# Kernel tuning notes

Measured on AMD Instinct MI355X. Metric: run time of the kernel, lower is better.

The kernel has to match this reference:

```python
import jax, jax.numpy as jnp
import numpy as np

ALPHA = 0.25
GAMMA = 2.0
MARGIN = 1.0
LAMBDA_GRAPH = 0.1
N = 8192
D = 128


def setup_inputs() -> dict:
    key = jax.random.key(0)
    k1, k2, k3, k4 = jax.random.split(key, 4)
    preds = jax.random.normal(k1, (N,), dtype=jnp.float32)
    targets = jax.random.randint(k2, (N,), 0, 2).astype(jnp.float32)  # binary labels
    features = jax.random.normal(k3, (N, D), dtype=jnp.float32)
    graph_features = jax.random.normal(k4, (N, D), dtype=jnp.float32)
    return {"preds": preds, "targets": targets, "features": features,
            "graph_features": graph_features}


def _focal_loss(preds, targets):
    # numerically stable BCE-with-logits, reduction='none'
    bce = jnp.maximum(preds, 0.0) - preds * targets + jnp.log1p(jnp.exp(-jnp.abs(preds)))
    pt = jnp.exp(-bce)
    return jnp.mean(ALPHA * (1.0 - pt) ** GAMMA * bce)


def _contrastive_loss(features, labels):
    # squared pairwise distances via ||a||^2 + ||b||^2 - 2 a.b  -> [N, N]
    sqn = jnp.sum(features * features, axis=-1)
    sq = sqn[:, None] + sqn[None, :] - 2.0 * (features @ features.T)
    sq = jnp.maximum(sq, 0.0)
    # safe sqrt (gradient-safe at 0)
    pos = sq > 0.0
    dist = jnp.where(pos, jnp.sqrt(jnp.where(pos, sq, 1.0)), 0.0)
    same = labels[:, None] == labels[None, :]
    # same-label pairs: dist^2 == sq ; different: clamp(margin - dist, 0)^2
    per_pair = jnp.where(same, sq, jnp.maximum(MARGIN - dist, 0.0) ** 2)
    return jnp.mean(per_pair)  # sum / N^2


def _graph_reg_loss(graph_features):
    diff = graph_features[1:] - graph_features[:-1]
    return jnp.mean(jnp.sqrt(jnp.sum(diff * diff, axis=1)))


def reference(preds, targets, features, graph_features):
    return (_focal_loss(preds, targets)
            + _contrastive_loss(features, targets)
            + LAMBDA_GRAPH * _graph_reg_loss(graph_features))
```

## Files before the change

kernel.cpp:

```cpp
#include <hip/hip_runtime.h>
#include <hip/hip_bf16.h>


#define N_PTS 8192
#define DIM 128

typedef __bf16 bf16x8 __attribute__((ext_vector_type(8)));
typedef float f32x4 __attribute__((ext_vector_type(4)));

#define VPART_OFF 0
#define SPART_OFF 131072
#define CPART_OFF 133120
#define FPART_OFF 166400
#define GPART_OFF 166912

#define NPAIR 2080
#define NFOCAL 32
#define NGRAPH 256
#define NMAIN (NPAIR + NFOCAL + NGRAPH)

__device__ __forceinline__ bf16x8 pack8(const float4 a, const float4 b) {
    bf16x8 r;
    r[0] = (__bf16)a.x; r[1] = (__bf16)a.y; r[2] = (__bf16)a.z; r[3] = (__bf16)a.w;
    r[4] = (__bf16)b.x; r[5] = (__bf16)b.y; r[6] = (__bf16)b.z; r[7] = (__bf16)b.w;
    return r;
}
__device__ __forceinline__ float ssq8(const float4 a, const float4 b) {
    return a.x * a.x + a.y * a.y + a.z * a.z + a.w * a.w
         + b.x * b.x + b.y * b.y + b.z * b.z + b.w * b.w;
}

__global__ __launch_bounds__(256) void prep_kernel(const float* __restrict__ feat,
                                                   const float* __restrict__ targets,
                                                   float* __restrict__ vpart,
                                                   float* __restrict__ spart) {
    const int b = blockIdx.x;
    const int tid = threadIdx.x;
    __shared__ float fA[512], f1[512];
    __shared__ float sred[4][3];
    const int w = tid >> 6, lane = tid & 63;
    const float2* feat2 = reinterpret_cast<const float2*>(feat);
    float2 accA = {0.f, 0.f}, acc1 = {0.f, 0.f};
    float ssqA = 0.f, ssq1 = 0.f, n1 = 0.f;
    int r = b * 64 + w * 16;
    #pragma unroll 4
    for (int i = 0; i < 16; ++i, ++r) {
        const float2 v = feat2[r * 64 + lane];
        const float tr = targets[r];
        accA.x += v.x; accA.y += v.y;
        acc1.x += tr * v.x; acc1.y += tr * v.y;
        const float s2 = v.x * v.x + v.y * v.y;
        ssqA += s2; ssq1 += tr * s2; n1 += tr;
    }
    fA[w * 128 + 2 * lane] = accA.x; fA[w * 128 + 2 * lane + 1] = accA.y;
    f1[w * 128 + 2 * lane] = acc1.x; f1[w * 128 + 2 * lane + 1] = acc1.y;
    #pragma unroll
    for (int off = 32; off > 0; off >>= 1) {
        ssqA += __shfl_down(ssqA, off);
        ssq1 += __shfl_down(ssq1, off);
    }
    if (lane == 0) { sred[w][0] = ssqA; sred[w][1] = ssq1; sred[w][2] = n1; }
    __syncthreads();
    if (tid < 128) {
        const int d = tid;
        const float c1 = f1[d] + f1[128 + d] + f1[256 + d] + f1[384 + d];
        const float ca = fA[d] + fA[128 + d] + fA[256 + d] + fA[384 + d];
        vpart[b * 256 + tid] = ca - c1;
    } else {
        const int d = tid - 128;
        vpart[b * 256 + tid] = f1[d] + f1[128 + d] + f1[256 + d] + f1[384 + d];
    }
    if (tid == 0) {
        float4 s;
        s.x = sred[0][0] + sred[1][0] + sred[2][0] + sred[3][0];
        s.y = sred[0][1] + sred[1][1] + sred[2][1] + sred[3][1];
        s.z = sred[0][2] + sred[1][2] + sred[2][2] + sred[3][2];
        s.w = 0.f;
        *reinterpret_cast<float4*>(spart + b * 4) = s;
    }
}

template<bool DIAG>
__device__ __forceinline__ float scan_slow(const f32x4 (&acc)[4][4],
                                           const f32x4 (&sqni)[4], const f32x4 (&ti4)[4],
                                           const float (&sqnj)[4], const float (&tj4)[4],
                                           int wm, int wn, int quad, int m15) {
    float lsum = 0.f;
    #pragma unroll
    for (int tm = 0; tm < 4; ++tm) {
        #pragma unroll
        for (int tn = 0; tn < 4; ++tn) {
            const int jl = wn * 64 + tn * 16 + m15;
            #pragma unroll
            for (int e = 0; e < 4; ++e) {
                const float sq = sqni[tm][e] + sqnj[tn] - 2.f * acc[tm][tn][e];
                bool excl = (ti4[tm][e] == tj4[tn]);
                if (DIAG) {
                    const int il = wm * 64 + tm * 16 + quad * 4 + e;
                    excl = excl || (jl <= il);
                }
                if (!excl && sq < 1.f) {
                    const float d = sqrtf(fmaxf(sq, 0.f));
                    const float m = 1.f - d;
                    lsum += 2.f * m * m;
                }
            }
        }
    }
    return lsum;
}

__global__ __launch_bounds__(256, 4) void main_kernel(const float* __restrict__ feat,
                                                      const float* __restrict__ preds,
                                                      const float* __restrict__ targets,
                                                      const float* __restrict__ gfeat,
                                                      float* __restrict__ c_part,
                                                      float* __restrict__ f_part,
                                                      float* __restrict__ g_part) {
    const int bx = blockIdx.x;
    const int tid = threadIdx.x;
    const int w = tid >> 6, lane = tid & 63;

    if (bx < NPAIR) {
        const int u = bx;
        const int vv = 2079 - u;
        int k = (int)((sqrtf(8.f * (float)vv + 1.f) - 1.f) * 0.5f);
        while ((k + 1) * (k + 2) / 2 <= vv) ++k;
        while (k * (k + 1) / 2 > vv) --k;
        const int bi = 63 - k;
        const int bj = 63 - (vv - k * (k + 1) / 2);

        const int quad = lane >> 4, m15 = lane & 15;
        const int wm = w >> 1, wn = w & 1;
        const int ibase = bi * 128 + wm * 64, jbase = bj * 128 + wn * 64;

        bf16x8 afs[4], bfs[4];
        float sA[4], sB[4];
        #pragma unroll
        for (int t = 0; t < 4; ++t) {
            const float* pa = feat + (ibase + t * 16 + m15) * DIM + 8 * quad;
            const float4 a0 = *reinterpret_cast<const float4*>(pa);
            const float4 a1 = *reinterpret_cast<const float4*>(pa + 4);
            afs[t] = pack8(a0, a1);
            float s = ssq8(a0, a1);
            s += __shfl_xor(s, 16); s += __shfl_xor(s, 32);
            sA[t] = s;
            const float* pb = feat + (jbase + t * 16 + m15) * DIM + 8 * quad;
            const float4 b0 = *reinterpret_cast<const float4*>(pb);
            const float4 b1 = *reinterpret_cast<const float4*>(pb + 4);
            bfs[t] = pack8(b0, b1);
            float sb = ssq8(b0, b1);
            sb += __shfl_xor(sb, 16); sb += __shfl_xor(sb, 32);
            sB[t] = sb;
        }
        f32x4 acc[4][4];
        #pragma unroll
        for (int a = 0; a < 4; ++a)
            #pragma unroll
            for (int b = 0; b < 4; ++b) acc[a][b] = (f32x4){0.f, 0.f, 0.f, 0.f};
        #pragma unroll
        for (int tm = 0; tm < 4; ++tm)
            #pragma unroll
            for (int tn = 0; tn < 4; ++tn)
                acc[tm][tn] = __builtin_amdgcn_mfma_f32_16x16x32_bf16(
                    afs[tm], bfs[tn], acc[tm][tn], 0, 0, 0);

        float minv = 1e30f;
        #pragma unroll
        for (int tm = 0; tm < 4; ++tm) {
            #pragma unroll
            for (int e = 0; e < 4; ++e) {
                const float sa = __shfl(sA[tm], quad * 4 + e);
                #pragma unroll
                for (int tn = 0; tn < 4; ++tn)
                    minv = fminf(minv, sa + sB[tn] - 2.f * acc[tm][tn][e]);
            }
        }

        float lsum = 0.f;
        if (__any(minv < 2.f)) {
            float qi = 0.f, qj = 0.f;
            {
                const float4* ri = reinterpret_cast<const float4*>(feat + (ibase + lane) * DIM);
                const float4* rj = reinterpret_cast<const float4*>(feat + (jbase + lane) * DIM);
                #pragma unroll 8
                for (int c2 = 0; c2 < 32; ++c2) {
                    const float4 x = ri[c2]; qi += x.x * x.x + x.y * x.y + x.z * x.z + x.w * x.w;
                    const float4 y = rj[c2]; qj += y.x * y.x + y.y * y.y + y.z * y.z + y.w * y.w;
                }
            }
            f32x4 sqni[4], ti4[4];
            float sqnj[4], tj4[4];
            #pragma unroll
            for (int tm = 0; tm < 4; ++tm) {
                #pragma unroll
                for (int e = 0; e < 4; ++e) sqni[tm][e] = __shfl(qi, tm * 16 + quad * 4 + e);
                ti4[tm] = *reinterpret_cast<const f32x4*>(targets + ibase + tm * 16 + quad * 4);
            }
            #pragma unroll
            for (int tn = 0; tn < 4; ++tn) {
                sqnj[tn] = __shfl(qj, tn * 16 + m15);
                tj4[tn] = targets[jbase + tn * 16 + m15];
            }
            for (int ks = 1; ks < 4; ++ks) {
                bf16x8 af2[4], bf2[4];
                #pragma unroll
                for (int t = 0; t < 4; ++t) {
                    const float* pa = feat + (ibase + t * 16 + m15) * DIM + 8 * (quad + 4 * ks);
                    af2[t] = pack8(*reinterpret_cast<const float4*>(pa),
                                   *reinterpret_cast<const float4*>(pa + 4));
                    const float* pb = feat + (jbase + t * 16 + m15) * DIM + 8 * (quad + 4 * ks);
                    bf2[t] = pack8(*reinterpret_cast<const float4*>(pb),
                                   *reinterpret_cast<const float4*>(pb + 4));
                }
                #pragma unroll
                for (int tm = 0; tm < 4; ++tm)
                    #pragma unroll
                    for (int tn = 0; tn < 4; ++tn)
                        acc[tm][tn] = __builtin_amdgcn_mfma_f32_16x16x32_bf16(
                            af2[tm], bf2[tn], acc[tm][tn], 0, 0, 0);
            }
            lsum = (bi == bj)
                ? scan_slow<true >(acc, sqni, ti4, sqnj, tj4, wm, wn, quad, m15)
                : scan_slow<false>(acc, sqni, ti4, sqnj, tj4, wm, wn, quad, m15);
            #pragma unroll
            for (int off = 32; off > 0; off >>= 1) lsum += __shfl_down(lsum, off);
        }
        if (lane == 0) c_part[u * 4 + w] = lsum;
    } else if (bx < NPAIR + NFOCAL) {
        const int b = bx - NPAIR;
        const int i = b * 256 + tid;
        const float p = preds[i], t = targets[i];
        const float bce = fmaxf(p, 0.f) - p * t + log1pf(expf(-fabsf(p)));
        const float pt = expf(-bce);
        const float om = 1.f - pt;
        float fv = 0.25f * om * om * bce;
        #pragma unroll
        for (int off = 32; off > 0; off >>= 1) fv += __shfl_down(fv, off);
        if (lane == 0) f_part[b * 4 + w] = fv;
    } else {
        const int b = bx - NPAIR - NFOCAL;
        float ga = 0.f;
        #pragma unroll
        for (int it = 0; it < 8; ++it) {
            const int r = b * 4 + w + it * 1024;
            if (r < N_PTS - 1) {
                const float2 a = *reinterpret_cast<const float2*>(gfeat + r * DIM + lane * 2);
                const float2 bb = *reinterpret_cast<const float2*>(gfeat + (r + 1) * DIM + lane * 2);
                const float dx = bb.x - a.x, dy = bb.y - a.y;
                float s = dx * dx + dy * dy;
                #pragma unroll
                for (int off = 32; off > 0; off >>= 1) s += __shfl_down(s, off);
                if (lane == 0) ga += sqrtf(s);
            }
        }
        if (lane == 0) g_part[b * 4 + w] = ga;
    }
}

__global__ __launch_bounds__(256) void finalize_kernel(const float* __restrict__ c_part,
                                                       const float* __restrict__ f_part,
                                                       const float* __restrict__ g_part,
                                                       const float* __restrict__ vpart,
                                                       const float* __restrict__ spart,
                                                       float* __restrict__ out) {
    __shared__ double sC[4], sF[4], sG[4], sV[4], sST[4], sS1[4], sN1[4];
    const int tid = threadIdx.x;
    const int w = tid >> 6, lane = tid & 63;

    double c = 0.0;
    for (int i = tid; i < NPAIR * 4; i += 256) c += (double)c_part[i];
    double f = (tid < NFOCAL * 4) ? (double)f_part[tid] : 0.0;
    double g = 0.0;
    for (int i = tid; i < NGRAPH * 4; i += 256) g += (double)g_part[i];

    float V = 0.f;
    #pragma unroll 8
    for (int b2 = 0; b2 < 128; ++b2) V += vpart[b2 * 256 + tid];
    double vsq = (double)V * (double)V;

    double st = 0.0, s1 = 0.0, n1 = 0.0;
    if (tid < 128) {
        const float4 s = *reinterpret_cast<const float4*>(spart + tid * 4);
        st = s.x; s1 = s.y; n1 = s.z;
    }
    #pragma unroll
    for (int off = 32; off > 0; off >>= 1) {
        c += __shfl_down(c, off);
        f += __shfl_down(f, off);
        g += __shfl_down(g, off);
        vsq += __shfl_down(vsq, off);
        st += __shfl_down(st, off);
        s1 += __shfl_down(s1, off);
        n1 += __shfl_down(n1, off);
    }
    if (lane == 0) {
        sC[w] = c; sF[w] = f; sG[w] = g; sV[w] = vsq;
        sST[w] = st; sS1[w] = s1; sN1[w] = n1;
    }
    __syncthreads();
    if (tid == 0) {
        const double cs = sC[0] + sC[1] + sC[2] + sC[3];
        const double fs = sF[0] + sF[1] + sF[2] + sF[3];
        const double gs = sG[0] + sG[1] + sG[2] + sG[3];
        const double v0sq = sV[0] + sV[1];
        const double v1sq = sV[2] + sV[3];
        const double stot = sST[0] + sST[1] + sST[2] + sST[3];
        const double s1s  = sS1[0] + sS1[1] + sS1[2] + sS1[3];
        const double n1s  = sN1[0] + sN1[1] + sN1[2] + sN1[3];
        const double n0s = (double)N_PTS - n1s;
        const double s0s = stot - s1s;
        const double same = 2.0 * (n0s * s0s - v0sq) + 2.0 * (n1s * s1s - v1sq);
        out[0] = (float)((cs + same) / ((double)N_PTS * (double)N_PTS)
                         + fs / (double)N_PTS
                         + 0.1 * (gs / (double)(N_PTS - 1)));
    }
}

extern "C" void kernel_launch(void* const* d_in, const int* in_sizes, int n_in,
                              void* d_out, int out_size, void* d_ws, size_t ws_size,
                              hipStream_t stream) {
    const float* preds    = (const float*)d_in[0];
    const float* targets  = (const float*)d_in[1];
    const float* features = (const float*)d_in[2];
    const float* gfeat    = (const float*)d_in[3];
    char* ws = (char*)d_ws;
    float* vpart  = (float*)(ws + VPART_OFF);
    float* spart  = (float*)(ws + SPART_OFF);
    float* c_part = (float*)(ws + CPART_OFF);
    float* f_part = (float*)(ws + FPART_OFF);
    float* g_part = (float*)(ws + GPART_OFF);
    float* out = (float*)d_out;

    prep_kernel<<<128, 256, 0, stream>>>(features, targets, vpart, spart);
    main_kernel<<<NMAIN, 256, 0, stream>>>(features, preds, targets, gfeat,
                                           c_part, f_part, g_part);
    finalize_kernel<<<1, 256, 0, stream>>>(c_part, f_part, g_part, vpart, spart, out);
}
```

Baseline: 123.8 us.

## Fold prep into main kernel and coarsen blocks to 8 tiles each

Result: slower. 149.6 us (+20.9%).

```diff
diff --git a/kernel.cpp b/kernel.cpp
--- a/kernel.cpp
+++ b/kernel.cpp
@@ -7,17 +7,18 @@
 
 typedef __bf16 bf16x8 __attribute__((ext_vector_type(8)));
 typedef float f32x4 __attribute__((ext_vector_type(4)));
+
+#define G_PAIR 260
+#define G_PREP 32
+#define G_FOCAL 4
+#define G_GRAPH 64
+#define NMAIN (G_PAIR + G_PREP + G_FOCAL + G_GRAPH)
 
 #define VPART_OFF 0
 #define SPART_OFF 131072
 #define CPART_OFF 133120
-#define FPART_OFF 166400
-#define GPART_OFF 166912
-
-#define NPAIR 2080
-#define NFOCAL 32
-#define NGRAPH 256
-#define NMAIN (NPAIR + NFOCAL + NGRAPH)
+#define FPART_OFF 137280
+#define GPART_OFF 137344
 
 __device__ __forceinline__ bf16x8 pack8(const float4 a, const float4 b) {
     bf16x8 r;
@@ -28,56 +29,6 @@
 __device__ __forceinline__ float ssq8(const float4 a, const float4 b) {
     return a.x * a.x + a.y * a.y + a.z * a.z + a.w * a.w
          + b.x * b.x + b.y * b.y + b.z * b.z + b.w * b.w;
-}
-
-__global__ __launch_bounds__(256) void prep_kernel(const float* __restrict__ feat,
-                                                   const float* __restrict__ targets,
-                                                   float* __restrict__ vpart,
-                                                   float* __restrict__ spart) {
-    const int b = blockIdx.x;
-    const int tid = threadIdx.x;
-    __shared__ float fA[512], f1[512];
-    __shared__ float sred[4][3];
-    const int w = tid >> 6, lane = tid & 63;
-    const float2* feat2 = reinterpret_cast<const float2*>(feat);
-    float2 accA = {0.f, 0.f}, acc1 = {0.f, 0.f};
-    float ssqA = 0.f, ssq1 = 0.f, n1 = 0.f;
-    int r = b * 64 + w * 16;
-    #pragma unroll 4
-    for (int i = 0; i < 16; ++i, ++r) {
-        const float2 v = feat2[r * 64 + lane];
-        const float tr = targets[r];
-        accA.x += v.x; accA.y += v.y;
-        acc1.x += tr * v.x; acc1.y += tr * v.y;
-        const float s2 = v.x * v.x + v.y * v.y;
-        ssqA += s2; ssq1 += tr * s2; n1 += tr;
-    }
-    fA[w * 128 + 2 * lane] = accA.x; fA[w * 128 + 2 * lane + 1] = accA.y;
-    f1[w * 128 + 2 * lane] = acc1.x; f1[w * 128 + 2 * lane + 1] = acc1.y;
-    #pragma unroll
-    for (int off = 32; off > 0; off >>= 1) {
-        ssqA += __shfl_down(ssqA, off);
-        ssq1 += __shfl_down(ssq1, off);
-    }
-    if (lane == 0) { sred[w][0] = ssqA; sred[w][1] = ssq1; sred[w][2] = n1; }
-    __syncthreads();
-    if (tid < 128) {
-        const int d = tid;
-        const float c1 = f1[d] + f1[128 + d] + f1[256 + d] + f1[384 + d];
-        const float ca = fA[d] + fA[128 + d] + fA[256 + d] + fA[384 + d];
-        vpart[b * 256 + tid] = ca - c1;
-    } else {
-        const int d = tid - 128;
-        vpart[b * 256 + tid] = f1[d] + f1[128 + d] + f1[256 + d] + f1[384 + d];
-    }
-    if (tid == 0) {
-        float4 s;
-        s.x = sred[0][0] + sred[1][0] + sred[2][0] + sred[3][0];
-        s.y = sred[0][1] + sred[1][1] + sred[2][1] + sred[3][1];
-        s.z = sred[0][2] + sred[1][2] + sred[2][2] + sred[3][2];
-        s.w = 0.f;
-        *reinterpret_cast<float4*>(spart + b * 4) = s;
-    }
 }
 
 template<bool DIAG>
@@ -114,144 +65,212 @@
                                                       const float* __restrict__ preds,
                                                       const float* __restrict__ targets,
                                                       const float* __restrict__ gfeat,
+                                                      float* __restrict__ vpart,
+                                                      float* __restrict__ spart,
                                                       float* __restrict__ c_part,
                                                       float* __restrict__ f_part,
                                                       float* __restrict__ g_part) {
+    __shared__ float fA[512], f1[512];
+    __shared__ float sred[4][3];
     const int bx = blockIdx.x;
     const int tid = threadIdx.x;
     const int w = tid >> 6, lane = tid & 63;
 
-    if (bx < NPAIR) {
-        const int u = bx;
-        const int vv = 2079 - u;
-        int k = (int)((sqrtf(8.f * (float)vv + 1.f) - 1.f) * 0.5f);
-        while ((k + 1) * (k + 2) / 2 <= vv) ++k;
-        while (k * (k + 1) / 2 > vv) --k;
-        const int bi = 63 - k;
-        const int bj = 63 - (vv - k * (k + 1) / 2);
-
+    if (bx < G_PAIR) {
         const int quad = lane >> 4, m15 = lane & 15;
         const int wm = w >> 1, wn = w & 1;
-        const int ibase = bi * 128 + wm * 64, jbase = bj * 128 + wn * 64;
-
-        bf16x8 afs[4], bfs[4];
-        float sA[4], sB[4];
-        #pragma unroll
-        for (int t = 0; t < 4; ++t) {
-            const float* pa = feat + (ibase + t * 16 + m15) * DIM + 8 * quad;
-            const float4 a0 = *reinterpret_cast<const float4*>(pa);
-            const float4 a1 = *reinterpret_cast<const float4*>(pa + 4);
-            afs[t] = pack8(a0, a1);
-            float s = ssq8(a0, a1);
-            s += __shfl_xor(s, 16); s += __shfl_xor(s, 32);
-            sA[t] = s;
-            const float* pb = feat + (jbase + t * 16 + m15) * DIM + 8 * quad;
-            const float4 b0 = *reinterpret_cast<const float4*>(pb);
-            const float4 b1 = *reinterpret_cast<const float4*>(pb + 4);
-            bfs[t] = pack8(b0, b1);
-            float sb = ssq8(b0, b1);
-            sb += __shfl_xor(sb, 16); sb += __shfl_xor(sb, 32);
-            sB[t] = sb;
-        }
-        f32x4 acc[4][4];
-        #pragma unroll
-        for (int a = 0; a < 4; ++a)
-            #pragma unroll
-            for (int b = 0; b < 4; ++b) acc[a][b] = (f32x4){0.f, 0.f, 0.f, 0.f};
-        #pragma unroll
-        for (int tm = 0; tm < 4; ++tm)
-            #pragma unroll
-            for (int tn = 0; tn < 4; ++tn)
-                acc[tm][tn] = __builtin_amdgcn_mfma_f32_16x16x32_bf16(
-                    afs[tm], bfs[tn], acc[tm][tn], 0, 0, 0);
-
-        float minv = 1e30f;
-        #pragma unroll
-        for (int tm = 0; tm < 4; ++tm) {
-            #pragma unroll
-            for (int e = 0; e < 4; ++e) {
-                const float sa = __shfl(sA[tm], quad * 4 + e);
+        float csum = 0.f;
+
+        for (int t8 = 0; t8 < 8; ++t8) {
+            const int u = bx * 8 + t8;
+            const int vv = 2079 - u;
+            int k = (int)((sqrtf(8.f * (float)vv + 1.f) - 1.f) * 0.5f);
+            while ((k + 1) * (k + 2) / 2 <= vv) ++k;
+            while (k * (k + 1) / 2 > vv) --k;
+            const int bi = 63 - k;
+            const int bj = 63 - (vv - k * (k + 1) / 2);
+            const int ibase = bi * 128 + wm * 64, jbase = bj * 128 + wn * 64;
+
+            bf16x8 afs[4], bfs[4];
+            float sA[4], sB[4];
+            #pragma unroll
+            for (int t = 0; t < 4; ++t) {
+                const float* pa = feat + (ibase + t * 16 + m15) * DIM + 8 * quad;
+                const float4 a0 = *reinterpret_cast<const float4*>(pa);
+                const float4 a1 = *reinterpret_cast<const float4*>(pa + 4);
+                afs[t] = pack8(a0, a1);
+                float s = ssq8(a0, a1);
+                s += __shfl_xor(s, 16); s += __shfl_xor(s, 32);
+                sA[t] = s;
+                const float* pb = feat + (jbase + t * 16 + m15) * DIM + 8 * quad;
+                const float4 b0 = *reinterpret_cast<const float4*>(pb);
+                const float4 b1 = *reinterpret_cast<const float4*>(pb + 4);
+                bfs[t] = pack8(b0, b1);
+                float sb = ssq8(b0, b1);
+                sb += __shfl_xor(sb, 16); sb += __shfl_xor(sb, 32);
+                sB[t] = sb;
+            }
+            f32x4 acc[4][4];
+            #pragma unroll
+            for (int a = 0; a < 4; ++a)
+                #pragma unroll
+                for (int b = 0; b < 4; ++b) acc[a][b] = (f32x4){0.f, 0.f, 0.f, 0.f};
+            #pragma unroll
+            for (int tm = 0; tm < 4; ++tm)
                 #pragma unroll
                 for (int tn = 0; tn < 4; ++tn)
-                    minv = fminf(minv, sa + sB[tn] - 2.f * acc[tm][tn][e]);
-            }
-        }
-
-        float lsum = 0.f;
-        if (__any(minv < 2.f)) {
-            float qi = 0.f, qj = 0.f;
-            {
-                const float4* ri = reinterpret_cast<const float4*>(feat + (ibase + lane) * DIM);
-                const float4* rj = reinterpret_cast<const float4*>(feat + (jbase + lane) * DIM);
-                #pragma unroll 8
-                for (int c2 = 0; c2 < 32; ++c2) {
-                    const float4 x = ri[c2]; qi += x.x * x.x + x.y * x.y + x.z * x.z + x.w * x.w;
-                    const float4 y = rj[c2]; qj += y.x * y.x + y.y * y.y + y.z * y.z + y.w * y.w;
-                }
-            }
-            f32x4 sqni[4], ti4[4];
-            float sqnj[4], tj4[4];
+                    acc[tm][tn] = __builtin_amdgcn_mfma_f32_16x16x32_bf16(
+                        afs[tm], bfs[tn], acc[tm][tn], 0, 0, 0);
+
+            float minv = 1e30f;
             #pragma unroll
             for (int tm = 0; tm < 4; ++tm) {
                 #pragma unroll
-                for (int e = 0; e < 4; ++e) sqni[tm][e] = __shfl(qi, tm * 16 + quad * 4 + e);
-                ti4[tm] = *reinterpret_cast<const f32x4*>(targets + ibase + tm * 16 + quad * 4);
-            }
-            #pragma unroll
-            for (int tn = 0; tn < 4; ++tn) {
-                sqnj[tn] = __shfl(qj, tn * 16 + m15);
-                tj4[tn] = targets[jbase + tn * 16 + m15];
-            }
-            for (int ks = 1; ks < 4; ++ks) {
-                bf16x8 af2[4], bf2[4];
-                #pragma unroll
-                for (int t = 0; t < 4; ++t) {
-                    const float* pa = feat + (ibase + t * 16 + m15) * DIM + 8 * (quad + 4 * ks);
-                    af2[t] = pack8(*reinterpret_cast<const float4*>(pa),
-                                   *reinterpret_cast<const float4*>(pa + 4));
-                    const float* pb = feat + (jbase + t * 16 + m15) * DIM + 8 * (quad + 4 * ks);
-                    bf2[t] = pack8(*reinterpret_cast<const float4*>(pb),
-                                   *reinterpret_cast<const float4*>(pb + 4));
-                }
-                #pragma unroll
-                for (int tm = 0; tm < 4; ++tm)
+                for (int e = 0; e < 4; ++e) {
+                    const float sa = __shfl(sA[tm], quad * 4 + e);
                     #pragma unroll
                     for (int tn = 0; tn < 4; ++tn)
-                        acc[tm][tn] = __builtin_amdgcn_mfma_f32_16x16x32_bf16(
-                            af2[tm], bf2[tn], acc[tm][tn], 0, 0, 0);
-            }
-            lsum = (bi == bj)
-                ? scan_slow<true >(acc, sqni, ti4, sqnj, tj4, wm, wn, quad, m15)
-                : scan_slow<false>(acc, sqni, ti4, sqnj, tj4, wm, wn, quad, m15);
-            #pragma unroll
-            for (int off = 32; off > 0; off >>= 1) lsum += __shfl_down(lsum, off);
-        }
-        if (lane == 0) c_part[u * 4 + w] = lsum;
-    } else if (bx < NPAIR + NFOCAL) {
-        const int b = bx - NPAIR;
-        const int i = b * 256 + tid;
-        const float p = preds[i], t = targets[i];
-        const float bce = fmaxf(p, 0.f) - p * t + log1pf(expf(-fabsf(p)));
-        const float pt = expf(-bce);
-        const float om = 1.f - pt;
-        float fv = 0.25f * om * om * bce;
+                        minv = fminf(minv, sa + sB[tn] - 2.f * acc[tm][tn][e]);
+                }
+            }
+
+            if (__any(minv < 2.f)) {
+                float qi = 0.f, qj = 0.f;
+                {
+                    const float4* ri = reinterpret_cast<const float4*>(feat + (ibase + lane) * DIM);
+                    const float4* rj = reinterpret_cast<const float4*>(feat + (jbase + lane) * DIM);
+                    #pragma unroll 8
+                    for (int c2 = 0; c2 < 32; ++c2) {
+                        const float4 x = ri[c2]; qi += x.x * x.x + x.y * x.y + x.z * x.z + x.w * x.w;
+                        const float4 y = rj[c2]; qj += y.x * y.x + y.y * y.y + y.z * y.z + y.w * y.w;
+                    }
+                }
+                f32x4 sqni[4], ti4[4];
+                float sqnj[4], tj4[4];
+                #pragma unroll
+                for (int tm = 0; tm < 4; ++tm) {
+                    #pragma unroll
+                    for (int e = 0; e < 4; ++e) sqni[tm][e] = __shfl(qi, tm * 16 + quad * 4 + e);
+                    ti4[tm] = *reinterpret_cast<const f32x4*>(targets + ibase + tm * 16 + quad * 4);
+                }
+                #pragma unroll
+                for (int tn = 0; tn < 4; ++tn) {
+                    sqnj[tn] = __shfl(qj, tn * 16 + m15);
+                    tj4[tn] = targets[jbase + tn * 16 + m15];
+                }
+                for (int ks = 1; ks < 4; ++ks) {
+                    bf16x8 af2[4], bf2[4];
+                    #pragma unroll
+                    for (int t = 0; t < 4; ++t) {
+                        const float* pa = feat + (ibase + t * 16 + m15) * DIM + 8 * (quad + 4 * ks);
+                        af2[t] = pack8(*reinterpret_cast<const float4*>(pa),
+                                       *reinterpret_cast<const float4*>(pa + 4));
+                        const float* pb = feat + (jbase + t * 16 + m15) * DIM + 8 * (quad + 4 * ks);
+                        bf2[t] = pack8(*reinterpret_cast<const float4*>(pb),
+                                       *reinterpret_cast<const float4*>(pb + 4));
+                    }
+                    #pragma unroll
+                    for (int tm = 0; tm < 4; ++tm)
+                        #pragma unroll
+                        for (int tn = 0; tn < 4; ++tn)
+                            acc[tm][tn] = __builtin_amdgcn_mfma_f32_16x16x32_bf16(
+                                af2[tm], bf2[tn], acc[tm][tn], 0, 0, 0);
+                }
+                csum += (bi == bj)
+                    ? scan_slow<true >(acc, sqni, ti4, sqnj, tj4, wm, wn, quad, m15)
+                    : scan_slow<false>(acc, sqni, ti4, sqnj, tj4, wm, wn, quad, m15);
+            }
+        }
+        #pragma unroll
+        for (int off = 32; off > 0; off >>= 1) csum += __shfl_down(csum, off);
+        if (lane == 0) c_part[bx * 4 + w] = csum;
+    } else if (bx < G_PAIR + G_PREP) {
+        const int pb = bx - G_PAIR;
+        const float2* feat2 = reinterpret_cast<const float2*>(feat);
+        for (int sub = 0; sub < 4; ++sub) {
+            const int b = pb * 4 + sub;
+            float2 accA = {0.f, 0.f}, acc1 = {0.f, 0.f};
+            float ssqA = 0.f, ssq1 = 0.f, n1 = 0.f;
+            int r = b * 64 + w * 16;
+            #pragma unroll 4
+            for (int i = 0; i < 16; ++i, ++r) {
+                const float2 v = feat2[r * 64 + lane];
+                const float tr = targets[r];
+                accA.x += v.x; accA.y += v.y;
+                acc1.x += tr * v.x; acc1.y += tr * v.y;
+                const float s2 = v.x * v.x + v.y * v.y;
+                ssqA += s2; ssq1 += tr * s2; n1 += tr;
+            }
+            fA[w * 128 + 2 * lane] = accA.x; fA[w * 128 + 2 * lane + 1] = accA.y;
+            f1[w * 128 + 2 * lane] = acc1.x; f1[w * 128 + 2 * lane + 1] = acc1.y;
+            #pragma unroll
+            for (int off = 32; off > 0; off >>= 1) {
+                ssqA += __shfl_down(ssqA, off);
+                ssq1 += __shfl_down(ssq1, off);
+            }
+            if (lane == 0) { sred[w][0] = ssqA; sred[w][1] = ssq1; sred[w][2] = n1; }
+            __syncthreads();
+            if (tid < 128) {
+                const int d = tid;
+                const float c1 = f1[d] + f1[128 + d] + f1[256 + d] + f1[384 + d];
+                const float ca = fA[d] + fA[128 + d] + fA[256 + d] + fA[384 + d];
+                vpart[b * 256 + tid] = ca - c1;
+            } else {
+                const int d = tid - 128;
+                vpart[b * 256 + tid] = f1[d] + f1[128 + d] + f1[256 + d] + f1[384 + d];
+            }
+            if (tid == 0) {
+                float4 s;
+                s.x = sred[0][0] + sred[1][0] + sred[2][0] + sred[3][0];
+                s.y = sred[0][1] + sred[1][1] + sred[2][1] + sred[3][1];
+                s.z = sred[0][2] + sred[1][2] + sred[2][2] + sred[3][2];
+                s.w = 0.f;
+                *reinterpret_cast<float4*>(spart + b * 4) = s;
+            }
+            __syncthreads();
+        }
+    } else if (bx < G_PAIR + G_PREP + G_FOCAL) {
+        const int b = bx - G_PAIR - G_PREP;
+        float fv = 0.f;
+        #pragma unroll
+        for (int it = 0; it < 8; ++it) {
+            const int i = b * 2048 + it * 256 + tid;
+            const float p = preds[i], t = targets[i];
+            const float bce = fmaxf(p, 0.f) - p * t + log1pf(expf(-fabsf(p)));
+            const float pt = expf(-bce);
+            const float om = 1.f - pt;
+            fv += 0.25f * om * om * bce;
+        }
         #pragma unroll
         for (int off = 32; off > 0; off >>= 1) fv += __shfl_down(fv, off);
         if (lane == 0) f_part[b * 4 + w] = fv;
     } else {
-        const int b = bx - NPAIR - NFOCAL;
+        const int b = bx - G_PAIR - G_PREP - G_FOCAL;
         float ga = 0.f;
-        #pragma unroll
         for (int it = 0; it < 8; ++it) {
-            const int r = b * 4 + w + it * 1024;
-            if (r < N_PTS - 1) {
-                const float2 a = *reinterpret_cast<const float2*>(gfeat + r * DIM + lane * 2);
-                const float2 bb = *reinterpret_cast<const float2*>(gfeat + (r + 1) * DIM + lane * 2);
-                const float dx = bb.x - a.x, dy = bb.y - a.y;
-                float s = dx * dx + dy * dy;
-                #pragma unroll
-                for (int off = 32; off > 0; off >>= 1) s += __shfl_down(s, off);
-                if (lane == 0) ga += sqrtf(s);
+            const int rbase = b * 128 + w * 32 + it * 4;
+            float s[4];
+            #pragma unroll
+            for (int q = 0; q < 4; ++q) {
+                const int r = rbase + q;
+                if (r < N_PTS - 1) {
+                    const float2 a = *reinterpret_cast<const float2*>(gfeat + r * DIM + lane * 2);
+                    const float2 bb = *reinterpret_cast<const float2*>(gfeat + (r + 1) * DIM + lane * 2);
+                    const float dx = bb.x - a.x, dy = bb.y - a.y;
+                    s[q] = dx * dx + dy * dy;
+                } else s[q] = 0.f;
+            }
+            #pragma unroll
+            for (int off = 32; off > 0; off >>= 1) {
+                s[0] += __shfl_down(s[0], off);
+                s[1] += __shfl_down(s[1], off);
+                s[2] += __shfl_down(s[2], off);
+                s[3] += __shfl_down(s[3], off);
+            }
+            if (lane == 0) {
+                #pragma unroll
+                for (int q = 0; q < 4; ++q)
+                    if (rbase + q < N_PTS - 1) ga += sqrtf(s[q]);
             }
         }
         if (lane == 0) g_part[b * 4 + w] = ga;
@@ -269,10 +288,9 @@
     const int w = tid >> 6, lane = tid & 63;
 
     double c = 0.0;
-    for (int i = tid; i < NPAIR * 4; i += 256) c += (double)c_part[i];
-    double f = (tid < NFOCAL * 4) ? (double)f_part[tid] : 0.0;
-    double g = 0.0;
-    for (int i = tid; i < NGRAPH * 4; i += 256) g += (double)g_part[i];
+    for (int i = tid; i < G_PAIR * 4; i += 256) c += (double)c_part[i];
+    double f = (tid < G_FOCAL * 4) ? (double)f_part[tid] : 0.0;
+    double g = (tid < G_GRAPH * 4) ? (double)g_part[tid] : 0.0;
 
     float V = 0.f;
     #pragma unroll 8
@@ -332,8 +350,7 @@
     float* g_part = (float*)(ws + GPART_OFF);
     float* out = (float*)d_out;
 
-    prep_kernel<<<128, 256, 0, stream>>>(features, targets, vpart, spart);
     main_kernel<<<NMAIN, 256, 0, stream>>>(features, preds, targets, gfeat,
-                                           c_part, f_part, g_part);
+                                           vpart, spart, c_part, f_part, g_part);
     finalize_kernel<<<1, 256, 0, stream>>>(c_part, f_part, g_part, vpart, spart, out);
 }
```

## Fold norms into MFMA screening tile via LDS and merge prep kernel

Applied to the files above, without the earlier changes.

Result: faster. 107.9 us (-12.8%).

```diff
diff --git a/kernel.cpp b/kernel.cpp
--- a/kernel.cpp
+++ b/kernel.cpp
@@ -7,6 +7,12 @@
 
 typedef __bf16 bf16x8 __attribute__((ext_vector_type(8)));
 typedef float f32x4 __attribute__((ext_vector_type(4)));
+
+#define NPAIR 2080
+#define NPREP 128
+#define NFOCAL 32
+#define NGRAPH 256
+#define NMAIN (NPAIR + NPREP + NFOCAL + NGRAPH)
 
 #define VPART_OFF 0
 #define SPART_OFF 131072
@@ -14,70 +20,33 @@
 #define FPART_OFF 166400
 #define GPART_OFF 166912
 
-#define NPAIR 2080
-#define NFOCAL 32
-#define NGRAPH 256
-#define NMAIN (NPAIR + NFOCAL + NGRAPH)
-
+#define LDS_BYTES (8192 + 8192 + 1024 + 1024)
+__device__ __forceinline__ int uoff(int g, int q, int m) {
+    return ((g * 4 + q) * 16 + m) * 16;
+}
+
+__device__ __forceinline__ float ssq4(const float4 a) {
+    return a.x * a.x + a.y * a.y + a.z * a.z + a.w * a.w;
+}
+__device__ __forceinline__ void store8(void* dst, float4 a, float4 b, float sc) {
+    union { __bf16 h[8]; uint4 u; } p;
+    p.h[0] = (__bf16)(sc * a.x); p.h[1] = (__bf16)(sc * a.y);
+    p.h[2] = (__bf16)(sc * a.z); p.h[3] = (__bf16)(sc * a.w);
+    p.h[4] = (__bf16)(sc * b.x); p.h[5] = (__bf16)(sc * b.y);
+    p.h[6] = (__bf16)(sc * b.z); p.h[7] = (__bf16)(sc * b.w);
+    *reinterpret_cast<uint4*>(dst) = p.u;
+}
+__device__ __forceinline__ void store4(void* dst, float4 a, float sc) {
+    union { __bf16 h[4]; uint2 u; } p;
+    p.h[0] = (__bf16)(sc * a.x); p.h[1] = (__bf16)(sc * a.y);
+    p.h[2] = (__bf16)(sc * a.z); p.h[3] = (__bf16)(sc * a.w);
+    *reinterpret_cast<uint2*>(dst) = p.u;
+}
 __device__ __forceinline__ bf16x8 pack8(const float4 a, const float4 b) {
     bf16x8 r;
     r[0] = (__bf16)a.x; r[1] = (__bf16)a.y; r[2] = (__bf16)a.z; r[3] = (__bf16)a.w;
     r[4] = (__bf16)b.x; r[5] = (__bf16)b.y; r[6] = (__bf16)b.z; r[7] = (__bf16)b.w;
     return r;
-}
-__device__ __forceinline__ float ssq8(const float4 a, const float4 b) {
-    return a.x * a.x + a.y * a.y + a.z * a.z + a.w * a.w
-         + b.x * b.x + b.y * b.y + b.z * b.z + b.w * b.w;
-}
-
-__global__ __launch_bounds__(256) void prep_kernel(const float* __restrict__ feat,
-                                                   const float* __restrict__ targets,
-                                                   float* __restrict__ vpart,
-                                                   float* __restrict__ spart) {
-    const int b = blockIdx.x;
-    const int tid = threadIdx.x;
-    __shared__ float fA[512], f1[512];
-    __shared__ float sred[4][3];
-    const int w = tid >> 6, lane = tid & 63;
-    const float2* feat2 = reinterpret_cast<const float2*>(feat);
-    float2 accA = {0.f, 0.f}, acc1 = {0.f, 0.f};
-    float ssqA = 0.f, ssq1 = 0.f, n1 = 0.f;
-    int r = b * 64 + w * 16;
-    #pragma unroll 4
-    for (int i = 0; i < 16; ++i, ++r) {
-        const float2 v = feat2[r * 64 + lane];
-        const float tr = targets[r];
-        accA.x += v.x; accA.y += v.y;
-        acc1.x += tr * v.x; acc1.y += tr * v.y;
-        const float s2 = v.x * v.x + v.y * v.y;
-        ssqA += s2; ssq1 += tr * s2; n1 += tr;
-    }
-    fA[w * 128 + 2 * lane] = accA.x; fA[w * 128 + 2 * lane + 1] = accA.y;
-    f1[w * 128 + 2 * lane] = acc1.x; f1[w * 128 + 2 * lane + 1] = acc1.y;
-    #pragma unroll
-    for (int off = 32; off > 0; off >>= 1) {
-        ssqA += __shfl_down(ssqA, off);
-        ssq1 += __shfl_down(ssq1, off);
-    }
-    if (lane == 0) { sred[w][0] = ssqA; sred[w][1] = ssq1; sred[w][2] = n1; }
-    __syncthreads();
-    if (tid < 128) {
-        const int d = tid;
-        const float c1 = f1[d] + f1[128 + d] + f1[256 + d] + f1[384 + d];
-        const float ca = fA[d] + fA[128 + d] + fA[256 + d] + fA[384 + d];
-        vpart[b * 256 + tid] = ca - c1;
-    } else {
-        const int d = tid - 128;
-        vpart[b * 256 + tid] = f1[d] + f1[128 + d] + f1[256 + d] + f1[384 + d];
-    }
-    if (tid == 0) {
-        float4 s;
-        s.x = sred[0][0] + sred[1][0] + sred[2][0] + sred[3][0];
-        s.y = sred[0][1] + sred[1][1] + sred[2][1] + sred[3][1];
-        s.z = sred[0][2] + sred[1][2] + sred[2][2] + sred[3][2];
-        s.w = 0.f;
-        *reinterpret_cast<float4*>(spart + b * 4) = s;
-    }
 }
 
 template<bool DIAG>
@@ -114,9 +83,12 @@
                                                       const float* __restrict__ preds,
                                                       const float* __restrict__ targets,
                                                       const float* __restrict__ gfeat,
+                                                      float* __restrict__ vpart,
+                                                      float* __restrict__ spart,
                                                       float* __restrict__ c_part,
                                                       float* __restrict__ f_part,
                                                       float* __restrict__ g_part) {
+    __shared__ __align__(16) char smem[LDS_BYTES];
     const int bx = blockIdx.x;
     const int tid = threadIdx.x;
     const int w = tid >> 6, lane = tid & 63;
@@ -132,26 +104,54 @@
 
         const int quad = lane >> 4, m15 = lane & 15;
         const int wm = w >> 1, wn = w & 1;
-        const int ibase = bi * 128 + wm * 64, jbase = bj * 128 + wn * 64;
+
+        char* Ap = smem;
+        char* Bp = smem + 8192;
+        float* s24A = reinterpret_cast<float*>(smem + 16384);
+        float* s24B = reinterpret_cast<float*>(smem + 17408);
+
+        {
+            const int r = tid >> 1, h = tid & 1;
+            const int g = r >> 4, m = r & 15;
+            const float4* f4 = reinterpret_cast<const float4*>(feat);
+            const int ab = (bi * 128 + r) * 32 + h * 3;
+            const int bb = (bj * 128 + r) * 32 + h * 3;
+            const float4 a0 = f4[ab], a1 = f4[ab + 1], a2 = f4[ab + 2];
+            const float4 b0 = f4[bb], b1 = f4[bb + 1], b2 = f4[bb + 2];
+            s24A[r * 2 + h] = ssq4(a0) + ssq4(a1) + ssq4(a2);
+            s24B[r * 2 + h] = ssq4(b0) + ssq4(b1) + ssq4(b2);
+            if (h == 0) {
+                store8(Ap + uoff(g, 0, m), a0, a1, -2.f);
+                store4(Ap + uoff(g, 1, m), a2, -2.f);
+                store8(Bp + uoff(g, 0, m), b0, b1, 1.f);
+                store4(Bp + uoff(g, 1, m), b2, 1.f);
+            } else {
+                store4(Ap + uoff(g, 1, m) + 8, a0, -2.f);
+                store8(Ap + uoff(g, 2, m), a1, a2, -2.f);
+                store4(Bp + uoff(g, 1, m) + 8, b0, 1.f);
+                store8(Bp + uoff(g, 2, m), b1, b2, 1.f);
+            }
+            __syncthreads();
+            if (tid < 128) {
+                const int rr = tid, gg = rr >> 4, mm = rr & 15;
+                const float sqa = s24A[rr * 2] + s24A[rr * 2 + 1];
+                const float sqb = s24B[rr * 2] + s24B[rr * 2 + 1];
+                union { __bf16 x[8]; uint4 u; } ua, ub;
+                #pragma unroll
+                for (int i = 0; i < 8; ++i) { ua.x[i] = (__bf16)0.f; ub.x[i] = (__bf16)0.f; }
+                ua.x[0] = (__bf16)sqa; ua.x[1] = (__bf16)1.f;
+                ub.x[0] = (__bf16)1.f; ub.x[1] = (__bf16)sqb;
+                *reinterpret_cast<uint4*>(Ap + uoff(gg, 3, mm)) = ua.u;
+                *reinterpret_cast<uint4*>(Bp + uoff(gg, 3, mm)) = ub.u;
+            }
+            __syncthreads();
+        }
 
         bf16x8 afs[4], bfs[4];
-        float sA[4], sB[4];
         #pragma unroll
         for (int t = 0; t < 4; ++t) {
-            const float* pa = feat + (ibase + t * 16 + m15) * DIM + 8 * quad;
-            const float4 a0 = *reinterpret_cast<const float4*>(pa);
-            const float4 a1 = *reinterpret_cast<const float4*>(pa + 4);
-            afs[t] = pack8(a0, a1);
-            float s = ssq8(a0, a1);
-            s += __shfl_xor(s, 16); s += __shfl_xor(s, 32);
-            sA[t] = s;
-            const float* pb = feat + (jbase + t * 16 + m15) * DIM + 8 * quad;
-            const float4 b0 = *reinterpret_cast<const float4*>(pb);
-            const float4 b1 = *reinterpret_cast<const float4*>(pb + 4);
-            bfs[t] = pack8(b0, b1);
-            float sb = ssq8(b0, b1);
-            sb += __shfl_xor(sb, 16); sb += __shfl_xor(sb, 32);
-            sB[t] = sb;
+            afs[t] = *reinterpret_cast<const bf16x8*>(Ap + uoff(wm * 4 + t, quad, m15));
+            bfs[t] = *reinterpret_cast<const bf16x8*>(Bp + uoff(wn * 4 + t, quad, m15));
         }
         f32x4 acc[4][4];
         #pragma unroll
@@ -167,18 +167,16 @@
 
         float minv = 1e30f;
         #pragma unroll
-        for (int tm = 0; tm < 4; ++tm) {
-            #pragma unroll
-            for (int e = 0; e < 4; ++e) {
-                const float sa = __shfl(sA[tm], quad * 4 + e);
-                #pragma unroll
-                for (int tn = 0; tn < 4; ++tn)
-                    minv = fminf(minv, sa + sB[tn] - 2.f * acc[tm][tn][e]);
-            }
-        }
+        for (int tm = 0; tm < 4; ++tm)
+            #pragma unroll
+            for (int tn = 0; tn < 4; ++tn)
+                #pragma unroll
+                for (int e = 0; e < 4; ++e)
+                    minv = fminf(minv, acc[tm][tn][e]);
 
         float lsum = 0.f;
         if (__any(minv < 2.f)) {
+            const int ibase = bi * 128 + wm * 64, jbase = bj * 128 + wn * 64;
             float qi = 0.f, qj = 0.f;
             {
                 const float4* ri = reinterpret_cast<const float4*>(feat + (ibase + lane) * DIM);
@@ -202,7 +200,11 @@
                 sqnj[tn] = __shfl(qj, tn * 16 + m15);
                 tj4[tn] = targets[jbase + tn * 16 + m15];
             }
-            for (int ks = 1; ks < 4; ++ks) {
+            #pragma unroll
+            for (int a = 0; a < 4; ++a)
+                #pragma unroll
+                for (int b = 0; b < 4; ++b) acc[a][b] = (f32x4){0.f, 0.f, 0.f, 0.f};
+            for (int ks = 0; ks < 4; ++ks) {
                 bf16x8 af2[4], bf2[4];
                 #pragma unroll
                 for (int t = 0; t < 4; ++t) {
@@ -227,8 +229,52 @@
             for (int off = 32; off > 0; off >>= 1) lsum += __shfl_down(lsum, off);
         }
         if (lane == 0) c_part[u * 4 + w] = lsum;
-    } else if (bx < NPAIR + NFOCAL) {
+    } else if (bx < NPAIR + NPREP) {
         const int b = bx - NPAIR;
+        float* fA = reinterpret_cast<float*>(smem);
+        float* f1 = reinterpret_cast<float*>(smem + 2048);
+        float (*sred)[3] = reinterpret_cast<float(*)[3]>(smem + 4096);
+        const float2* feat2 = reinterpret_cast<const float2*>(feat);
+        float2 accA = {0.f, 0.f}, acc1 = {0.f, 0.f};
+        float ssqA = 0.f, ssq1 = 0.f, n1 = 0.f;
+        int r = b * 64 + w * 16;
+        #pragma unroll 4
+        for (int i = 0; i < 16; ++i, ++r) {
+            const float2 v = feat2[r * 64 + lane];
+            const float tr = targets[r];
+            accA.x += v.x; accA.y += v.y;
+            acc1.x += tr * v.x; acc1.y += tr * v.y;
+            const float s2 = v.x * v.x + v.y * v.y;
+            ssqA += s2; ssq1 += tr * s2; n1 += tr;
+        }
+        fA[w * 128 + 2 * lane] = accA.x; fA[w * 128 + 2 * lane + 1] = accA.y;
+        f1[w * 128 + 2 * lane] = acc1.x; f1[w * 128 + 2 * lane + 1] = acc1.y;
+        #pragma unroll
+        for (int off = 32; off > 0; off >>= 1) {
+            ssqA += __shfl_down(ssqA, off);
+            ssq1 += __shfl_down(ssq1, off);
+        }
+        if (lane == 0) { sred[w][0] = ssqA; sred[w][1] = ssq1; sred[w][2] = n1; }
+        __syncthreads();
+        if (tid < 128) {
+            const int d = tid;
+            const float c1 = f1[d] + f1[128 + d] + f1[256 + d] + f1[384 + d];
+            const float ca = fA[d] + fA[128 + d] + fA[256 + d] + fA[384 + d];
+            vpart[b * 256 + tid] = ca - c1;
+        } else {
+            const int d = tid - 128;
+            vpart[b * 256 + tid] = f1[d] + f1[128 + d] + f1[256 + d] + f1[384 + d];
+        }
+        if (tid == 0) {
+            float4 s;
+            s.x = sred[0][0] + sred[1][0] + sred[2][0] + sred[3][0];
+            s.y = sred[0][1] + sred[1][1] + sred[2][1] + sred[3][1];
+            s.z = sred[0][2] + sred[1][2] + sred[2][2] + sred[3][2];
+            s.w = 0.f;
+            *reinterpret_cast<float4*>(spart + b * 4) = s;
+        }
+    } else if (bx < NPAIR + NPREP + NFOCAL) {
+        const int b = bx - NPAIR - NPREP;
         const int i = b * 256 + tid;
         const float p = preds[i], t = targets[i];
         const float bce = fmaxf(p, 0.f) - p * t + log1pf(expf(-fabsf(p)));
@@ -239,7 +285,7 @@
         for (int off = 32; off > 0; off >>= 1) fv += __shfl_down(fv, off);
         if (lane == 0) f_part[b * 4 + w] = fv;
     } else {
-        const int b = bx - NPAIR - NFOCAL;
+        const int b = bx - NPAIR - NPREP - NFOCAL;
         float ga = 0.f;
         #pragma unroll
         for (int it = 0; it < 8; ++it) {
@@ -332,8 +378,7 @@
     float* g_part = (float*)(ws + GPART_OFF);
     float* out = (float*)d_out;
 
-    prep_kernel<<<128, 256, 0, stream>>>(features, targets, vpart, spart);
     main_kernel<<<NMAIN, 256, 0, stream>>>(features, preds, targets, gfeat,
-                                           c_part, f_part, g_part);
+                                           vpart, spart, c_part, f_part, g_part);
     finalize_kernel<<<1, 256, 0, stream>>>(c_part, f_part, g_part, vpart, spart, out);
 }
```
